# Kernel tuning notes

Measured on AMD Instinct MI355X. Metric: run time of the kernel, lower is better.

The kernel has to match this reference:

```python
import jax, jax.numpy as jnp
import numpy as np

N, F, K, FP = 4096, 256, 8, 64  # nodes, in-feat, heads, out-feat per head
NEG_SLOPE = 0.2
MASK_FILL = -1e30  # stand-in for -inf (numerically safe under softmax/vjp)


def setup_inputs() -> dict:
    key = jax.random.key(0)
    k1, k2, k3, k4, k5 = jax.random.split(key, 5)
    x = jax.random.normal(k1, (N, F), dtype=jnp.float32)
    mask = jax.random.randint(k2, (1, N, N), 0, 2).astype(bool)
    idx = jnp.arange(N)
    mask = mask.at[0, idx, idx].set(True)  # self-loops guarantee no empty softmax rows
    W_w = jax.random.normal(k3, (K * FP, F), dtype=jnp.float32) * (1.0 / np.sqrt(F))
    W_b = jnp.zeros((K * FP,), dtype=jnp.float32)
    a_left = jax.random.normal(k4, (1, K, FP), dtype=jnp.float32) * 0.1
    a_right = jax.random.normal(k5, (1, K, FP), dtype=jnp.float32) * 0.1
    return {"x": x, "W_w": W_w, "W_b": W_b, "a_left": a_left, "a_right": a_right, "mask": mask}


def reference(x, W_w, W_b, a_left, a_right, mask):
    k, fp = a_left.shape[1], a_left.shape[2]
    # W(x): (N, K*F') -> (N, K, F')   [dropout p=0.0 -> identity]
    xe = (x @ W_w.T + W_b).reshape(-1, k, fp)
    # additive scores: h_left (K,N,1) + h_right (K,1,N) -> e (K,N,N)
    hl = jnp.einsum('nkf,kf->kn', xe, a_left[0])
    hr = jnp.einsum('nkf,kf->kn', xe, a_right[0])
    e = hl[:, :, None] + hr[:, None, :]
    e = jnp.where(e > 0, e, NEG_SLOPE * e)          # LeakyReLU(0.2)
    e = jnp.where(mask, e, MASK_FILL)               # masked_fill(~mask, -inf)
    a = jax.nn.softmax(e, axis=-1)                  # (K,N,N)
    # weighted sum of neighbor features: (K,N,N) x (N,K,F') -> (N,K,F')
    h_prime = jnp.einsum('knm,mkf->nkf', a, xe)
    h_prime = jax.nn.elu(h_prime)
    # non-final layer: elu again (as in source) then concat heads
    out = jax.nn.elu(h_prime).reshape(-1, k * fp)   # (N, K*F')
    return (out, mask)
```

## Files before the change

### kernel.cpp

```cpp
#include <hip/hip_runtime.h>
#include <hip/hip_bf16.h>

#define N_NODES 4096
#define F_IN    256
#define KH      8
#define KF      512
#define NEG_SLOPE 0.2f
#define EBIAS   4.0f

typedef _Float16 half8v __attribute__((ext_vector_type(8)));
typedef _Float16 half2v __attribute__((ext_vector_type(2)));
typedef __attribute__((ext_vector_type(4))) float floatx4;

union H8U4 { half8v v; unsigned u[4]; };

__device__ __forceinline__ unsigned short f2h(float f) {
    _Float16 h = (_Float16)f;
    unsigned short u; __builtin_memcpy(&u, &h, 2);
    return u;
}
__device__ __forceinline__ half2v asH2(unsigned u) {
    half2v h; __builtin_memcpy(&h, &u, 4);
    return h;
}
__device__ __forceinline__ unsigned asU(half2v h) {
    unsigned u; __builtin_memcpy(&u, &h, 4);
    return u;
}

__global__ __launch_bounds__(256) void mask_fused(
    const int* __restrict__ mask, float* __restrict__ outm,
    unsigned long long* __restrict__ bits) {
  const size_t base = (size_t)blockIdx.x * 1024;
  const int tid = threadIdx.x;
  #pragma unroll
  for (int c = 0; c < 4; ++c) {
    const size_t e = base + c * 256 + tid;
    const int v = mask[e];
    outm[e] = v ? 1.f : 0.f;
    const unsigned long long b = __ballot(v != 0);
    if ((tid & 63) == 0) {
      const size_t w = e >> 6;
      bits[(w & 63) * (size_t)N_NODES + (w >> 6)] = b;
    }
  }
}

__global__ __launch_bounds__(256) void mask_pack(
    const int* __restrict__ mask, unsigned long long* __restrict__ bits) {
  const size_t idx = (size_t)blockIdx.x * 256 + threadIdx.x;
  const unsigned long long b = __ballot(mask[idx] != 0);
  if ((threadIdx.x & 63) == 0) {
    const size_t w = idx >> 6;
    bits[(w & 63) * (size_t)N_NODES + (w >> 6)] = b;
  }
}
__global__ __launch_bounds__(256) void mask_copy(
    const int* __restrict__ mask, float* __restrict__ outm) {
  const size_t i4 = (size_t)blockIdx.x * 256 + threadIdx.x;
  const int4 mv = ((const int4*)mask)[i4];
  float4 o;
  o.x = mv.x ? 1.f : 0.f; o.y = mv.y ? 1.f : 0.f;
  o.z = mv.z ? 1.f : 0.f; o.w = mv.w ? 1.f : 0.f;
  ((float4*)outm)[i4] = o;
}

__global__ __launch_bounds__(256) void xe_gemm(
    const float* __restrict__ x,
    const float* __restrict__ Ww,
    const float* __restrict__ Wb,
    const float* __restrict__ al,
    const float* __restrict__ ar,
    unsigned short* __restrict__ xeB,
    float* __restrict__ hl,
    unsigned* __restrict__ EA,
    unsigned* __restrict__ EB,
    float* __restrict__ bmax) {
  __shared__ float As[32][65];
  __shared__ float Bs[32][65];
  __shared__ float redmax[4];
  const int tid = threadIdx.x;
  const int n0 = blockIdx.x * 64;
  const int j0 = blockIdx.y * 64;
  const int lr = tid >> 2;
  const int lc = (tid & 3) * 8;
  const int ty = tid >> 4;
  const int tx = tid & 15;
  float c[4][4];
  #pragma unroll
  for (int i = 0; i < 4; ++i)
    #pragma unroll
    for (int j = 0; j < 4; ++j) c[i][j] = 0.f;

  for (int f0 = 0; f0 < F_IN; f0 += 32) {
    const float* ap = x  + (size_t)(n0 + lr) * F_IN + f0 + lc;
    const float* bp = Ww + (size_t)(j0 + lr) * F_IN + f0 + lc;
    const float4 a0 = *(const float4*)ap;
    const float4 a1 = *(const float4*)(ap + 4);
    const float4 b0 = *(const float4*)bp;
    const float4 b1 = *(const float4*)(bp + 4);
    __syncthreads();
    As[lc + 0][lr] = a0.x; As[lc + 1][lr] = a0.y;
    As[lc + 2][lr] = a0.z; As[lc + 3][lr] = a0.w;
    As[lc + 4][lr] = a1.x; As[lc + 5][lr] = a1.y;
    As[lc + 6][lr] = a1.z; As[lc + 7][lr] = a1.w;
    Bs[lc + 0][lr] = b0.x; Bs[lc + 1][lr] = b0.y;
    Bs[lc + 2][lr] = b0.z; Bs[lc + 3][lr] = b0.w;
    Bs[lc + 4][lr] = b1.x; Bs[lc + 5][lr] = b1.y;
    Bs[lc + 6][lr] = b1.z; Bs[lc + 7][lr] = b1.w;
    __syncthreads();
    #pragma unroll
    for (int kk = 0; kk < 32; ++kk) {
      const float4 av = *(const float4*)&As[kk][ty * 4];
      const float4 bv = *(const float4*)&Bs[kk][tx * 4];
      const float a4[4] = {av.x, av.y, av.z, av.w};
      const float b4[4] = {bv.x, bv.y, bv.z, bv.w};
      #pragma unroll
      for (int i = 0; i < 4; ++i)
        #pragma unroll
        for (int j = 0; j < 4; ++j) c[i][j] = fmaf(a4[i], b4[j], c[i][j]);
    }
  }
  const float4 wb4 = *(const float4*)(Wb + j0 + tx * 4);
  const float4 al4 = *(const float4*)(al + j0 + tx * 4);
  const float4 ar4 = *(const float4*)(ar + j0 + tx * 4);
  const float wb[4] = {wb4.x, wb4.y, wb4.z, wb4.w};
  const float alv[4] = {al4.x, al4.y, al4.z, al4.w};
  const float arv[4] = {ar4.x, ar4.y, ar4.z, ar4.w};
  float v[4][4];
  float pl[4], pr[4];
  #pragma unroll
  for (int i = 0; i < 4; ++i) {
    float sl = 0.f, sr = 0.f;
    #pragma unroll
    for (int j = 0; j < 4; ++j) {
      v[i][j] = c[i][j] + wb[j];
      sl = fmaf(v[i][j], alv[j], sl);
      sr = fmaf(v[i][j], arv[j], sr);
    }
    pl[i] = sl; pr[i] = sr;
  }
  {
    const int k   = blockIdx.y;
    const int ft  = tx >> 2;
    const int fb  = (tx & 3) * 4;
    const int cc  = blockIdx.x;
    const int h_  = ty >> 3;
    const int qd  = (ty >> 1) & 3;
    const int jj0 = (ty & 1) * 4;
    unsigned short* tile = xeB + ((((size_t)(k * 4 + ft)) * 64 + cc) << 10)
                         + h_ * 512 + qd * 8 + jj0;
    #pragma unroll
    for (int j = 0; j < 4; ++j) {
      ushort4 pk;
      pk.x = f2h(v[0][j]); pk.y = f2h(v[1][j]);
      pk.z = f2h(v[2][j]); pk.w = f2h(v[3][j]);
      *(ushort4*)(tile + (fb + j) * 32) = pk;
    }
  }
  #pragma unroll
  for (int off = 8; off > 0; off >>= 1) {
    #pragma unroll
    for (int i = 0; i < 4; ++i) {
      pl[i] += __shfl_down(pl[i], off);
      pr[i] += __shfl_down(pr[i], off);
    }
  }
  if (tx == 0) {
    const int k = blockIdx.y;
    float4 o0 = {pl[0], pl[1], pl[2], pl[3]};
    *(float4*)(hl + k * N_NODES + n0 + ty * 4) = o0;
    unsigned short e1[4], e2[4];
    #pragma unroll
    for (int i = 0; i < 4; ++i) {
      e1[i] = f2h(__expf(pr[i] - EBIAS));
      e2[i] = f2h(__expf(NEG_SLOPE * (pr[i] - EBIAS)));
    }
    uint2 wa, wbv;
    wa.x  = (unsigned)e1[0] | ((unsigned)e1[1] << 16);
    wa.y  = (unsigned)e1[2] | ((unsigned)e1[3] << 16);
    wbv.x = (unsigned)e2[0] | ((unsigned)e2[1] << 16);
    wbv.y = (unsigned)e2[2] | ((unsigned)e2[3] << 16);
    *(uint2*)(EA + k * 2048 + ((n0 + ty * 4) >> 1)) = wa;
    *(uint2*)(EB + k * 2048 + ((n0 + ty * 4) >> 1)) = wbv;
  }
  float bm = (tx == 0)
      ? fmaxf(fmaxf(pr[0], pr[1]), fmaxf(pr[2], pr[3])) : -1e30f;
  bm = fmaxf(bm, __shfl_xor(bm, 16));
  bm = fmaxf(bm, __shfl_xor(bm, 32));
  if ((tid & 63) == 0) redmax[tid >> 6] = bm;
  __syncthreads();
  if (tid == 0) {
    bmax[blockIdx.y * 64 + blockIdx.x] =
        fmaxf(fmaxf(redmax[0], redmax[1]), fmaxf(redmax[2], redmax[3]));
  }
}

__global__ __launch_bounds__(256, 4) void gat_attn(
    const unsigned long long* __restrict__ mbitsT,
    const float* __restrict__ hl,
    const float* __restrict__ bmax,
    const unsigned* __restrict__ EA,
    const unsigned* __restrict__ EB,
    const unsigned short* __restrict__ xeB,
    float* __restrict__ out) {
  __shared__ float lds_acc[4][64][20];
  const int t = threadIdx.x;
  const int w4 = t >> 6;
  const int lane = t & 63;
  const int k  = blockIdx.x >> 8;
  const int rg = blockIdx.x & 255;
  const int n0 = rg * 16;
  const int row = lane & 15;
  const int quad = lane >> 4;
  const int q8 = quad * 8;

  float hm = bmax[k * 64 + lane];
  #pragma unroll
  for (int o = 1; o < 64; o <<= 1) hm = fmaxf(hm, __shfl_xor(hm, o));

  const float hlv = hl[k * N_NODES + n0 + row];
  const float sM = hlv + hm;
  const float Mv = fmaxf(sM, NEG_SLOPE * sM);
  const float c1f = __expf(hlv + EBIAS - Mv);
  const float c2f = __expf(NEG_SLOPE * (hlv + EBIAS) - Mv);
  const half2v c1h2 = {(_Float16)c1f, (_Float16)c1f};
  const half2v c2h2 = {(_Float16)c2f, (_Float16)c2f};

  const int c0 = w4 * 16;
  const int cEnd = c0 + 16;

  const unsigned* pEA = EA + k * 2048 + c0 * 32 + quad * 4;
  const unsigned* pEB = EB + k * 2048 + c0 * 32 + quad * 4;
  const unsigned long long* pM = mbitsT + (size_t)c0 * N_NODES + n0 + row;
  const unsigned short* pB = xeB + (((size_t)k * 4) << 16)
                           + ((size_t)c0 << 10) + row * 32 + q8;

  half8v ones;
  #pragma unroll
  for (int i = 0; i < 8; ++i) ones[i] = (_Float16)1.0f;

  floatx4 acc[4];
  #pragma unroll
  for (int ft = 0; ft < 4; ++ft) acc[ft] = (floatx4){0.f, 0.f, 0.f, 0.f};
  floatx4 accdp = (floatx4){0.f, 0.f, 0.f, 0.f};

  uint4 pA0 = *(const uint4*)pEA;
  uint4 pA1 = *(const uint4*)(pEA + 16);
  uint4 pB0 = *(const uint4*)pEB;
  uint4 pB1 = *(const uint4*)(pEB + 16);
  unsigned long long pMv = *pM;

  for (int cc = c0; cc < cEnd; ++cc) {
    half8v b0, b1, b2, b3, b4, b5, b6, b7;
    b0 = *(const half8v*)pB;                     b1 = *(const half8v*)(pB + 512);
    b2 = *(const half8v*)(pB + (64 << 10));      b3 = *(const half8v*)(pB + (64 << 10) + 512);
    b4 = *(const half8v*)(pB + (128 << 10));     b5 = *(const half8v*)(pB + (128 << 10) + 512);
    b6 = *(const half8v*)(pB + (192 << 10));     b7 = *(const half8v*)(pB + (192 << 10) + 512);
    pB += 1024;
    const uint4 eA0 = pA0, eA1 = pA1, eB0 = pB0, eB1 = pB1;
    const unsigned long long mb = pMv;
    pEA += 32; pEB += 32; pM += N_NODES;
    if (cc + 1 < cEnd) {
      pA0 = *(const uint4*)pEA;
      pA1 = *(const uint4*)(pEA + 16);
      pB0 = *(const uint4*)pEB;
      pB1 = *(const uint4*)(pEB + 16);
      pMv = *pM;
    }
    const unsigned mlo = (unsigned)(mb >> q8);
    const unsigned mhi = (unsigned)(mb >> (32 + q8));
    H8U4 a0, a1;
    {
      const unsigned ea[4] = {eA0.x, eA0.y, eA0.z, eA0.w};
      const unsigned eb[4] = {eB0.x, eB0.y, eB0.z, eB0.w};
      #pragma unroll
      for (int p = 0; p < 4; ++p) {
        const half2v w2 = __builtin_elementwise_max(c1h2 * asH2(ea[p]),
                                                    c2h2 * asH2(eb[p]));
        const unsigned tb = mlo >> (2 * p);
        const unsigned sel = (((tb & 1u) | ((tb & 2u) << 15)) * 0xFFFFu);
        a0.u[p] = asU(w2) & sel;
      }
    }
    {
      const unsigned ea[4] = {eA1.x, eA1.y, eA1.z, eA1.w};
      const unsigned eb[4] = {eB1.x, eB1.y, eB1.z, eB1.w};
      #pragma unroll
      for (int p = 0; p < 4; ++p) {
        const half2v w2 = __builtin_elementwise_max(c1h2 * asH2(ea[p]),
                                                    c2h2 * asH2(eb[p]));
        const unsigned tb = mhi >> (2 * p);
        const unsigned sel = (((tb & 1u) | ((tb & 2u) << 15)) * 0xFFFFu);
        a1.u[p] = asU(w2) & sel;
      }
    }
    accdp = __builtin_amdgcn_mfma_f32_16x16x32_f16(a0.v, ones, accdp, 0, 0, 0);
    accdp = __builtin_amdgcn_mfma_f32_16x16x32_f16(a1.v, ones, accdp, 0, 0, 0);
    acc[0] = __builtin_amdgcn_mfma_f32_16x16x32_f16(a0.v, b0, acc[0], 0, 0, 0);
    acc[0] = __builtin_amdgcn_mfma_f32_16x16x32_f16(a1.v, b1, acc[0], 0, 0, 0);
    acc[1] = __builtin_amdgcn_mfma_f32_16x16x32_f16(a0.v, b2, acc[1], 0, 0, 0);
    acc[1] = __builtin_amdgcn_mfma_f32_16x16x32_f16(a1.v, b3, acc[1], 0, 0, 0);
    acc[2] = __builtin_amdgcn_mfma_f32_16x16x32_f16(a0.v, b4, acc[2], 0, 0, 0);
    acc[2] = __builtin_amdgcn_mfma_f32_16x16x32_f16(a1.v, b5, acc[2], 0, 0, 0);
    acc[3] = __builtin_amdgcn_mfma_f32_16x16x32_f16(a0.v, b6, acc[3], 0, 0, 0);
    acc[3] = __builtin_amdgcn_mfma_f32_16x16x32_f16(a1.v, b7, acc[3], 0, 0, 0);
  }

  #pragma unroll
  for (int i = 0; i < 16; ++i) lds_acc[w4][lane][i] = acc[i >> 2][i & 3];
  #pragma unroll
  for (int i = 0; i < 4; ++i) lds_acc[w4][lane][16 + i] = accdp[i];
  __syncthreads();

  #pragma unroll
  for (int j = 0; j < 4; ++j) {
    const int sl = 4 * w4 + j;
    const int row_o = quad * 4 + j;
    float fa = 0.f, dpt = 0.f;
    #pragma unroll
    for (int w2 = 0; w2 < 4; ++w2) {
      fa  += lds_acc[w2][lane][sl];
      dpt += lds_acc[w2][lane][16 + j];
    }
    float v = fa / dpt;
    v = (v > 0.f) ? v : (__expf(v) - 1.f);
    v = (v > 0.f) ? v : (__expf(v) - 1.f);
    out[(size_t)(n0 + row_o) * KF + k * 64 + w4 * 16 + row] = v;
  }
}

extern "C" void kernel_launch(void* const* d_in, const int* in_sizes, int n_in,
                              void* d_out, int out_size, void* d_ws, size_t ws_size,
                              hipStream_t stream) {
  const float* x    = (const float*)d_in[0];
  const float* Ww   = (const float*)d_in[1];
  const float* Wb   = (const float*)d_in[2];
  const float* al   = (const float*)d_in[3];
  const float* ar   = (const float*)d_in[4];
  const int*   mask = (const int*)d_in[5];

  float* out      = (float*)d_out;
  float* out_mask = out + (size_t)N_NODES * KF;

  const bool use_ws = (ws_size >= (8u << 20));
  char* scratch = use_ws ? (char*)d_ws : (char*)out_mask;
  unsigned short* xeB  = (unsigned short*)scratch;
  float*          hl   = (float*)(scratch + (4u << 20));
  unsigned*       EA   = (unsigned*)(hl + KH * N_NODES);
  unsigned*       EB   = EA + KH * 2048;
  float*          bmax = (float*)(EB + KH * 2048);
  unsigned long long* mbitsT = (unsigned long long*)(scratch + (5u << 20));

  dim3 ga(N_NODES / 64, KF / 64);
  xe_gemm<<<ga, 256, 0, stream>>>(x, Ww, Wb, al, ar, xeB, hl, EA, EB, bmax);

  if (use_ws) {
    mask_fused<<<(N_NODES * (size_t)N_NODES) / 1024, 256, 0, stream>>>(
        mask, out_mask, mbitsT);
    gat_attn<<<256 * KH, 256, 0, stream>>>(mbitsT, hl, bmax, EA, EB, xeB, out);
  } else {
    mask_pack<<<(N_NODES * (size_t)N_NODES) / 256, 256, 0, stream>>>(mask, mbitsT);
    gat_attn<<<256 * KH, 256, 0, stream>>>(mbitsT, hl, bmax, EA, EB, xeB, out);
    mask_copy<<<(N_NODES * (size_t)N_NODES) / (4 * 256), 256, 0, stream>>>(mask, out_mask);
  }
}
```

Measured before the change: 242.6 us.

## Process two 16-row tiles per attention block and coalesce packed mask writes

The attention kernel now handles 32 destination rows per block as two 16-row sub-tiles. Each loaded xe B-fragment and edge-score vector is reused for both sub-tiles, halving global B traffic per output row. In exchange it doubles accumulator registers, which may lower occupancy, and halves the grid size. The mask packing kernel now tiles 64x64 and stages ballot words in LDS, so the transposed bit matrix is written as contiguous 64-word runs instead of scattered 8-byte stores.

```diff
diff --git a/kernel.cpp b/kernel.cpp
--- a/kernel.cpp
+++ b/kernel.cpp
@@ -31,19 +31,24 @@
 __global__ __launch_bounds__(256) void mask_fused(
     const int* __restrict__ mask, float* __restrict__ outm,
     unsigned long long* __restrict__ bits) {
-  const size_t base = (size_t)blockIdx.x * 1024;
+  __shared__ unsigned long long wbuf[64];
   const int tid = threadIdx.x;
-  #pragma unroll
-  for (int c = 0; c < 4; ++c) {
-    const size_t e = base + c * 256 + tid;
+  const int w4 = tid >> 6;
+  const int lane = tid & 63;
+  const int cb = blockIdx.x & 63;
+  const int n0 = (blockIdx.x >> 6) * 64;
+  const int colb = cb * 64;
+  #pragma unroll
+  for (int r = 0; r < 16; ++r) {
+    const int row = n0 + w4 * 16 + r;
+    const size_t e = (size_t)row * N_NODES + colb + lane;
     const int v = mask[e];
     outm[e] = v ? 1.f : 0.f;
     const unsigned long long b = __ballot(v != 0);
-    if ((tid & 63) == 0) {
-      const size_t w = e >> 6;
-      bits[(w & 63) * (size_t)N_NODES + (w >> 6)] = b;
-    }
-  }
+    if (lane == 0) wbuf[w4 * 16 + r] = b;
+  }
+  __syncthreads();
+  if (tid < 64) bits[(size_t)cb * N_NODES + n0 + tid] = wbuf[tid];
 }
 
 __global__ __launch_bounds__(256) void mask_pack(
@@ -208,9 +213,9 @@
   const int t = threadIdx.x;
   const int w4 = t >> 6;
   const int lane = t & 63;
-  const int k  = blockIdx.x >> 8;
-  const int rg = blockIdx.x & 255;
-  const int n0 = rg * 16;
+  const int k  = blockIdx.x >> 7;
+  const int rg = blockIdx.x & 127;
+  const int n0 = rg * 32;
   const int row = lane & 15;
   const int quad = lane >> 4;
   const int q8 = quad * 8;
@@ -219,13 +224,21 @@
   #pragma unroll
   for (int o = 1; o < 64; o <<= 1) hm = fmaxf(hm, __shfl_xor(hm, o));
 
-  const float hlv = hl[k * N_NODES + n0 + row];
-  const float sM = hlv + hm;
-  const float Mv = fmaxf(sM, NEG_SLOPE * sM);
-  const float c1f = __expf(hlv + EBIAS - Mv);
-  const float c2f = __expf(NEG_SLOPE * (hlv + EBIAS) - Mv);
-  const half2v c1h2 = {(_Float16)c1f, (_Float16)c1f};
-  const half2v c2h2 = {(_Float16)c2f, (_Float16)c2f};
+  const float* hlp = hl + k * N_NODES + n0 + row;
+  const float hlA = hlp[0];
+  const float hlB = hlp[16];
+  const float sA = hlA + hm;
+  const float MA = fmaxf(sA, NEG_SLOPE * sA);
+  const float sB = hlB + hm;
+  const float MB = fmaxf(sB, NEG_SLOPE * sB);
+  const float c1Af = __expf(hlA + EBIAS - MA);
+  const float c2Af = __expf(NEG_SLOPE * (hlA + EBIAS) - MA);
+  const float c1Bf = __expf(hlB + EBIAS - MB);
+  const float c2Bf = __expf(NEG_SLOPE * (hlB + EBIAS) - MB);
+  const half2v c1A = {(_Float16)c1Af, (_Float16)c1Af};
+  const half2v c2A = {(_Float16)c2Af, (_Float16)c2Af};
+  const half2v c1B = {(_Float16)c1Bf, (_Float16)c1Bf};
+  const half2v c2B = {(_Float16)c2Bf, (_Float16)c2Bf};
 
   const int c0 = w4 * 16;
   const int cEnd = c0 + 16;
@@ -240,16 +253,21 @@
   #pragma unroll
   for (int i = 0; i < 8; ++i) ones[i] = (_Float16)1.0f;
 
-  floatx4 acc[4];
-  #pragma unroll
-  for (int ft = 0; ft < 4; ++ft) acc[ft] = (floatx4){0.f, 0.f, 0.f, 0.f};
-  floatx4 accdp = (floatx4){0.f, 0.f, 0.f, 0.f};
+  floatx4 accA[4], accB[4];
+  #pragma unroll
+  for (int ft = 0; ft < 4; ++ft) {
+    accA[ft] = (floatx4){0.f, 0.f, 0.f, 0.f};
+    accB[ft] = (floatx4){0.f, 0.f, 0.f, 0.f};
+  }
+  floatx4 dpA = (floatx4){0.f, 0.f, 0.f, 0.f};
+  floatx4 dpB = (floatx4){0.f, 0.f, 0.f, 0.f};
 
   uint4 pA0 = *(const uint4*)pEA;
   uint4 pA1 = *(const uint4*)(pEA + 16);
   uint4 pB0 = *(const uint4*)pEB;
   uint4 pB1 = *(const uint4*)(pEB + 16);
-  unsigned long long pMv = *pM;
+  unsigned long long pMvA = pM[0];
+  unsigned long long pMvB = pM[16];
 
   for (int cc = c0; cc < cEnd; ++cc) {
     half8v b0, b1, b2, b3, b4, b5, b6, b7;
@@ -259,64 +277,88 @@
     b6 = *(const half8v*)(pB + (192 << 10));     b7 = *(const half8v*)(pB + (192 << 10) + 512);
     pB += 1024;
     const uint4 eA0 = pA0, eA1 = pA1, eB0 = pB0, eB1 = pB1;
-    const unsigned long long mb = pMv;
+    const unsigned long long mbA = pMvA, mbB = pMvB;
     pEA += 32; pEB += 32; pM += N_NODES;
     if (cc + 1 < cEnd) {
       pA0 = *(const uint4*)pEA;
       pA1 = *(const uint4*)(pEA + 16);
       pB0 = *(const uint4*)pEB;
       pB1 = *(const uint4*)(pEB + 16);
-      pMv = *pM;
-    }
-    const unsigned mlo = (unsigned)(mb >> q8);
-    const unsigned mhi = (unsigned)(mb >> (32 + q8));
-    H8U4 a0, a1;
+      pMvA = pM[0];
+      pMvB = pM[16];
+    }
+    const unsigned ea_lo[4] = {eA0.x, eA0.y, eA0.z, eA0.w};
+    const unsigned eb_lo[4] = {eB0.x, eB0.y, eB0.z, eB0.w};
+    const unsigned ea_hi[4] = {eA1.x, eA1.y, eA1.z, eA1.w};
+    const unsigned eb_hi[4] = {eB1.x, eB1.y, eB1.z, eB1.w};
     {
-      const unsigned ea[4] = {eA0.x, eA0.y, eA0.z, eA0.w};
-      const unsigned eb[4] = {eB0.x, eB0.y, eB0.z, eB0.w};
+      const unsigned mlo = (unsigned)(mbA >> q8);
+      const unsigned mhi = (unsigned)(mbA >> (32 + q8));
+      H8U4 a0, a1;
       #pragma unroll
       for (int p = 0; p < 4; ++p) {
-        const half2v w2 = __builtin_elementwise_max(c1h2 * asH2(ea[p]),
-                                                    c2h2 * asH2(eb[p]));
+        const half2v w2 = __builtin_elementwise_max(c1A * asH2(ea_lo[p]),
+                                                    c2A * asH2(eb_lo[p]));
         const unsigned tb = mlo >> (2 * p);
-        const unsigned sel = (((tb & 1u) | ((tb & 2u) << 15)) * 0xFFFFu);
-        a0.u[p] = asU(w2) & sel;
+        a0.u[p] = asU(w2) & (((tb & 1u) | ((tb & 2u) << 15)) * 0xFFFFu);
       }
-    }
-    {
-      const unsigned ea[4] = {eA1.x, eA1.y, eA1.z, eA1.w};
-      const unsigned eb[4] = {eB1.x, eB1.y, eB1.z, eB1.w};
       #pragma unroll
       for (int p = 0; p < 4; ++p) {
-        const half2v w2 = __builtin_elementwise_max(c1h2 * asH2(ea[p]),
-                                                    c2h2 * asH2(eb[p]));
+        const half2v w2 = __builtin_elementwise_max(c1A * asH2(ea_hi[p]),
+                                                    c2A * asH2(eb_hi[p]));
         const unsigned tb = mhi >> (2 * p);
-        const unsigned sel = (((tb & 1u) | ((tb & 2u) << 15)) * 0xFFFFu);
-        a1.u[p] = asU(w2) & sel;
+        a1.u[p] = asU(w2) & (((tb & 1u) | ((tb & 2u) << 15)) * 0xFFFFu);
       }
-    }
-    accdp = __builtin_amdgcn_mfma_f32_16x16x32_f16(a0.v, ones, accdp, 0, 0, 0);
-    accdp = __builtin_amdgcn_mfma_f32_16x16x32_f16(a1.v, ones, accdp, 0, 0, 0);
-    acc[0] = __builtin_amdgcn_mfma_f32_16x16x32_f16(a0.v, b0, acc[0], 0, 0, 0);
-    acc[0] = __builtin_amdgcn_mfma_f32_16x16x32_f16(a1.v, b1, acc[0], 0, 0, 0);
-    acc[1] = __builtin_amdgcn_mfma_f32_16x16x32_f16(a0.v, b2, acc[1], 0, 0, 0);
-    acc[1] = __builtin_amdgcn_mfma_f32_16x16x32_f16(a1.v, b3, acc[1], 0, 0, 0);
-    acc[2] = __builtin_amdgcn_mfma_f32_16x16x32_f16(a0.v, b4, acc[2], 0, 0, 0);
-    acc[2] = __builtin_amdgcn_mfma_f32_16x16x32_f16(a1.v, b5, acc[2], 0, 0, 0);
-    acc[3] = __builtin_amdgcn_mfma_f32_16x16x32_f16(a0.v, b6, acc[3], 0, 0, 0);
-    acc[3] = __builtin_amdgcn_mfma_f32_16x16x32_f16(a1.v, b7, acc[3], 0, 0, 0);
-  }
-
-  #pragma unroll
-  for (int i = 0; i < 16; ++i) lds_acc[w4][lane][i] = acc[i >> 2][i & 3];
-  #pragma unroll
-  for (int i = 0; i < 4; ++i) lds_acc[w4][lane][16 + i] = accdp[i];
+      dpA = __builtin_amdgcn_mfma_f32_16x16x32_f16(a0.v, ones, dpA, 0, 0, 0);
+      dpA = __builtin_amdgcn_mfma_f32_16x16x32_f16(a1.v, ones, dpA, 0, 0, 0);
+      accA[0] = __builtin_amdgcn_mfma_f32_16x16x32_f16(a0.v, b0, accA[0], 0, 0, 0);
+      accA[0] = __builtin_amdgcn_mfma_f32_16x16x32_f16(a1.v, b1, accA[0], 0, 0, 0);
+      accA[1] = __builtin_amdgcn_mfma_f32_16x16x32_f16(a0.v, b2, accA[1], 0, 0, 0);
+      accA[1] = __builtin_amdgcn_mfma_f32_16x16x32_f16(a1.v, b3, accA[1], 0, 0, 0);
+      accA[2] = __builtin_amdgcn_mfma_f32_16x16x32_f16(a0.v, b4, accA[2], 0, 0, 0);
+      accA[2] = __builtin_amdgcn_mfma_f32_16x16x32_f16(a1.v, b5, accA[2], 0, 0, 0);
+      accA[3] = __builtin_amdgcn_mfma_f32_16x16x32_f16(a0.v, b6, accA[3], 0, 0, 0);
+      accA[3] = __builtin_amdgcn_mfma_f32_16x16x32_f16(a1.v, b7, accA[3], 0, 0, 0);
+    }
+    {
+      const unsigned mlo = (unsigned)(mbB >> q8);
+      const unsigned mhi = (unsigned)(mbB >> (32 + q8));
+      H8U4 a0, a1;
+      #pragma unroll
+      for (int p = 0; p < 4; ++p) {
+        const half2v w2 = __builtin_elementwise_max(c1B * asH2(ea_lo[p]),
+                                                    c2B * asH2(eb_lo[p]));
+        const unsigned tb = mlo >> (2 * p);
+        a0.u[p] = asU(w2) & (((tb & 1u) | ((tb & 2u) << 15)) * 0xFFFFu);
+      }
+      #pragma unroll
+      for (int p = 0; p < 4; ++p) {
+        const half2v w2 = __builtin_elementwise_max(c1B * asH2(ea_hi[p]),
+                                                    c2B * asH2(eb_hi[p]));
+        const unsigned tb = mhi >> (2 * p);
+        a1.u[p] = asU(w2) & (((tb & 1u) | ((tb & 2u) << 15)) * 0xFFFFu);
+      }
+      dpB = __builtin_amdgcn_mfma_f32_16x16x32_f16(a0.v, ones, dpB, 0, 0, 0);
+      dpB = __builtin_amdgcn_mfma_f32_16x16x32_f16(a1.v, ones, dpB, 0, 0, 0);
+      accB[0] = __builtin_amdgcn_mfma_f32_16x16x32_f16(a0.v, b0, accB[0], 0, 0, 0);
+      accB[0] = __builtin_amdgcn_mfma_f32_16x16x32_f16(a1.v, b1, accB[0], 0, 0, 0);
+      accB[1] = __builtin_amdgcn_mfma_f32_16x16x32_f16(a0.v, b2, accB[1], 0, 0, 0);
+      accB[1] = __builtin_amdgcn_mfma_f32_16x16x32_f16(a1.v, b3, accB[1], 0, 0, 0);
+      accB[2] = __builtin_amdgcn_mfma_f32_16x16x32_f16(a0.v, b4, accB[2], 0, 0, 0);
+      accB[2] = __builtin_amdgcn_mfma_f32_16x16x32_f16(a1.v, b5, accB[2], 0, 0, 0);
+      accB[3] = __builtin_amdgcn_mfma_f32_16x16x32_f16(a0.v, b6, accB[3], 0, 0, 0);
+      accB[3] = __builtin_amdgcn_mfma_f32_16x16x32_f16(a1.v, b7, accB[3], 0, 0, 0);
+    }
+  }
+
+  #pragma unroll
+  for (int i = 0; i < 16; ++i) lds_acc[w4][lane][i] = accA[i >> 2][i & 3];
+  #pragma unroll
+  for (int i = 0; i < 4; ++i) lds_acc[w4][lane][16 + i] = dpA[i];
   __syncthreads();
-
   #pragma unroll
   for (int j = 0; j < 4; ++j) {
     const int sl = 4 * w4 + j;
-    const int row_o = quad * 4 + j;
     float fa = 0.f, dpt = 0.f;
     #pragma unroll
     for (int w2 = 0; w2 < 4; ++w2) {
@@ -326,7 +368,27 @@
     float v = fa / dpt;
     v = (v > 0.f) ? v : (__expf(v) - 1.f);
     v = (v > 0.f) ? v : (__expf(v) - 1.f);
-    out[(size_t)(n0 + row_o) * KF + k * 64 + w4 * 16 + row] = v;
+    out[(size_t)(n0 + quad * 4 + j) * KF + k * 64 + w4 * 16 + row] = v;
+  }
+  __syncthreads();
+  #pragma unroll
+  for (int i = 0; i < 16; ++i) lds_acc[w4][lane][i] = accB[i >> 2][i & 3];
+  #pragma unroll
+  for (int i = 0; i < 4; ++i) lds_acc[w4][lane][16 + i] = dpB[i];
+  __syncthreads();
+  #pragma unroll
+  for (int j = 0; j < 4; ++j) {
+    const int sl = 4 * w4 + j;
+    float fa = 0.f, dpt = 0.f;
+    #pragma unroll
+    for (int w2 = 0; w2 < 4; ++w2) {
+      fa  += lds_acc[w2][lane][sl];
+      dpt += lds_acc[w2][lane][16 + j];
+    }
+    float v = fa / dpt;
+    v = (v > 0.f) ? v : (__expf(v) - 1.f);
+    v = (v > 0.f) ? v : (__expf(v) - 1.f);
+    out[(size_t)(n0 + 16 + quad * 4 + j) * KF + k * 64 + w4 * 16 + row] = v;
   }
 }
 
@@ -356,12 +418,11 @@
   xe_gemm<<<ga, 256, 0, stream>>>(x, Ww, Wb, al, ar, xeB, hl, EA, EB, bmax);
 
   if (use_ws) {
-    mask_fused<<<(N_NODES * (size_t)N_NODES) / 1024, 256, 0, stream>>>(
-        mask, out_mask, mbitsT);
-    gat_attn<<<256 * KH, 256, 0, stream>>>(mbitsT, hl, bmax, EA, EB, xeB, out);
+    mask_fused<<<64 * 64, 256, 0, stream>>>(mask, out_mask, mbitsT);
+    gat_attn<<<128 * KH, 256, 0, stream>>>(mbitsT, hl, bmax, EA, EB, xeB, out);
   } else {
     mask_pack<<<(N_NODES * (size_t)N_NODES) / 256, 256, 0, stream>>>(mask, mbitsT);
-    gat_attn<<<256 * KH, 256, 0, stream>>>(mbitsT, hl, bmax, EA, EB, xeB, out);
+    gat_attn<<<128 * KH, 256, 0, stream>>>(mbitsT, hl, bmax, EA, EB, xeB, out);
     mask_copy<<<(N_NODES * (size_t)N_NODES) / (4 * 256), 256, 0, stream>>>(mask, out_mask);
   }
 }
```

Measured after the change: 258.1 us. 1.06x slower.
